# Optimization experiments

Hardware: AMD Instinct MI355X
Metric: run time of the kernel (lower is better)

Reference implementation:

```python
import jax, jax.numpy as jnp
import numpy as np

N_NODES = 32768
N_EDGES = 131072
BATCH = 512
SEQ_LEN = 1000
VOCAB = 26  # vocab_size=25 + 1 padding row
EMB = 128


def _bn(x, g, b):
    # BatchNorm1d forward with batch statistics (training-mode math), eps=1e-5
    m = x.mean(0)
    v = x.var(0)
    return g * (x - m) * jax.lax.rsqrt(v + 1e-5) + b


def _gcn(x, src, dst, W, b, n):
    deg = 1.0 + jax.ops.segment_sum(jnp.ones(src.shape[0], x.dtype), dst, num_segments=n)
    dis = jax.lax.rsqrt(deg)
    xw = x @ W
    msg = xw[src] * (dis[src] * dis[dst])[:, None]
    agg = jax.ops.segment_sum(msg, dst, num_segments=n) + xw * (dis * dis)[:, None]
    return agg + b


def _conv1d(x, k, b, pad):
    # x: [B, C_in, L], k: [C_out, C_in, K]
    y = jax.lax.conv_general_dilated(x, k, (1,), [(pad, pad)],
                                     dimension_numbers=('NCH', 'OIH', 'NCH'))
    return y + b[None, :, None]


def setup_inputs() -> dict:
    key = jax.random.key(0)
    ks = jax.random.split(key, 32)
    f = lambda i, shape, s=0.1: (jax.random.normal(ks[i], shape, dtype=jnp.float32) * s)
    inp = {
        'x': jax.random.normal(ks[0], (N_NODES, 5), dtype=jnp.float32),
        'edge_index': jax.random.randint(ks[1], (2, N_EDGES), 0, N_NODES, dtype=jnp.int32),
        'batch': jnp.sort(jax.random.randint(ks[2], (N_NODES,), 0, BATCH, dtype=jnp.int32)),
        'protein_seq': jax.random.randint(ks[3], (BATCH, SEQ_LEN), 0, VOCAB, dtype=jnp.int32),
        # GCN weights
        'W1': f(4, (5, 64)), 'b1': f(5, (64,)),
        'g1': jnp.ones((64,)), 'bt1': jnp.zeros((64,)),
        'W2': f(6, (64, 128)), 'b2': f(7, (128,)),
        'g2': jnp.ones((128,)), 'bt2': jnp.zeros((128,)),
        'W3': f(8, (128, 128)), 'b3': f(9, (128,)),
        'g3': jnp.ones((128,)), 'bt3': jnp.zeros((128,)),
        # protein embedding (row 0 = padding_idx, zeroed)
        'emb': f(10, (VOCAB, EMB)).at[0].set(0.0),
        # protein convs
        'ck1': f(11, (32, 128, 4)), 'cb1': f(12, (32,)),
        'ck2': f(13, (64, 32, 6)), 'cb2': f(14, (64,)),
        'ck3': f(15, (96, 64, 8)), 'cb3': f(16, (96,)),
        'fw1': f(17, (224, 512)), 'fb1': f(18, (512,)),
        'fw2': f(19, (512, 256)), 'fb2': f(20, (256,)),
        'fw3': f(21, (256, 1)), 'fb3': f(22, (1,)),
    }
    return inp


def reference(x, edge_index, batch, protein_seq,
              W1, b1, g1, bt1, W2, b2, g2, bt2, W3, b3, g3, bt3,
              emb, ck1, cb1, ck2, cb2, ck3, cb3,
              fw1, fb1, fw2, fb2, fw3, fb3):
    src, dst = edge_index[0], edge_index[1]
    relu = jax.nn.relu
    # Drug GNN encoder
    h = relu(_bn(_gcn(x, src, dst, W1, b1, N_NODES), g1, bt1))
    h = relu(_bn(_gcn(h, src, dst, W2, b2, N_NODES), g2, bt2))
    h = relu(_bn(_gcn(h, src, dst, W3, b3, N_NODES), g3, bt3))
    cnt = jax.ops.segment_sum(jnp.ones(N_NODES, h.dtype), batch, num_segments=BATCH)
    drug_emb = jax.ops.segment_sum(h, batch, num_segments=BATCH) / jnp.maximum(cnt, 1.0)[:, None]
    # Protein CNN encoder
    e = emb[protein_seq]                    # [B, L, 128]
    p = jnp.transpose(e, (0, 2, 1))         # [B, 128, L]
    p = relu(_conv1d(p, ck1, cb1, 1))       # [B, 32, 999]
    p = relu(_conv1d(p, ck2, cb2, 2))       # [B, 64, 998]
    p = relu(_conv1d(p, ck3, cb3, 3))       # [B, 96, 997]
    prot_emb = p.max(axis=2)                # [B, 96]
    c = jnp.concatenate([drug_emb, prot_emb], axis=1)  # [B, 224]
    c = relu(c @ fw1 + fb1)
    c = relu(c @ fw2 + fb2)
    out = (c @ fw3 + fb3)[:, 0]             # [B]
    return out
```

## Files before the change

### kernel.cpp

```cpp
#include <hip/hip_runtime.h>

#define NN 32768
#define NE 131072
#define NB 512
#define SL 1000

using bf16x8 = __attribute__((ext_vector_type(8))) short;
using f32x4  = __attribute__((ext_vector_type(4))) float;

static __device__ __forceinline__ unsigned short f2b(float f) {
  union { float f; unsigned u; } x; x.f = f;
  unsigned r = x.u + 0x7fffu + ((x.u >> 16) & 1u);
  return (unsigned short)(r >> 16);
}

static __device__ __forceinline__ void bn_from_raw(float sum, float ssq, float g, float b,
                                                   float& sc, float& sh) {
  float m = sum / 32768.f;
  float v = ssq / 32768.f - m * m;
  sc = g * rsqrtf(v + 1e-5f);
  sh = b - m * sc;
}

__global__ void k_degprep(const int* __restrict__ dst, int* __restrict__ degi,
                          const float* __restrict__ emb, const float* __restrict__ ck1,
                          const float* __restrict__ ck2, const float* __restrict__ ck3,
                          unsigned short* __restrict__ emb_bf, unsigned short* __restrict__ wt1,
                          unsigned short* __restrict__ wt2, unsigned short* __restrict__ wt3) {
  int gid = blockIdx.x * 256 + threadIdx.x;
  atomicAdd(&degi[dst[gid]], 1);
  int idx = gid;
  if (idx < 3328) {
    emb_bf[idx] = f2b(emb[idx]);
  } else if (idx < 3328 + 16384) {
    int i = idx - 3328;
    int kt = i >> 12, co = (i >> 7) & 31, ci = i & 127;
    wt1[i] = f2b(ck1[co * 512 + ci * 4 + kt]);
  } else if (idx < 3328 + 16384 + 12288) {
    int i = idx - 3328 - 16384;
    int kt = i >> 11, co = (i >> 5) & 63, ci = i & 31;
    wt2[i] = f2b(ck2[co * 192 + ci * 6 + kt]);
  } else if (idx < 3328 + 16384 + 12288 + 49152) {
    int i = idx - 3328 - 16384 - 12288;
    int kt = i / 6144, co = (i >> 6) % 96, ci = i & 63;
    wt3[i] = f2b(ck3[co * 512 + ci * 8 + kt]);
  }
}

__global__ void k_scan(const int* __restrict__ degi, int* __restrict__ base,
                       int* __restrict__ cursor, float* __restrict__ dis) {
  __shared__ int part[1024];
  int tid = threadIdx.x;
  int v[32];
  int s = 0;
  int lo = tid * 32;
#pragma unroll
  for (int i = 0; i < 32; ++i) { v[i] = degi[lo + i]; s += v[i]; }
  part[tid] = s;
  __syncthreads();
  for (int off = 1; off < 1024; off <<= 1) {
    int val = (tid >= off) ? part[tid - off] : 0;
    __syncthreads();
    part[tid] += val;
    __syncthreads();
  }
  int run = (tid > 0) ? part[tid - 1] : 0;
#pragma unroll
  for (int i = 0; i < 32; ++i) {
    base[lo + i] = run;
    cursor[lo + i] = run;
    dis[lo + i] = rsqrtf(1.0f + (float)v[i]);
    run += v[i];
  }
  if (tid == 1023) base[NN] = run;
}

__global__ void k_fill(const int* __restrict__ src, const int* __restrict__ dst,
                       int* __restrict__ cursor, unsigned short* __restrict__ csr_src, int E) {
  int e = blockIdx.x * 256 + threadIdx.x;
  if (e < E) {
    int d = dst[e];
    int pos = atomicAdd(&cursor[d], 1);
    csr_src[pos] = (unsigned short)src[e];
  }
}

__launch_bounds__(256)
__global__ void k_gfc1s(const float* __restrict__ x, const float* __restrict__ dis,
                        const int* __restrict__ base, const unsigned short* __restrict__ csr_src,
                        const float* __restrict__ W1, float* __restrict__ out,
                        float* __restrict__ st) {
  __shared__ float sW[5][64];
  __shared__ float a5[256][6];
  __shared__ float red[16][64];
  int tid = threadIdx.x;
  for (int i = tid; i < 320; i += 256) sW[i >> 6][i & 63] = W1[i];
  int n = blockIdx.x * 256 + tid;
  float dn = dis[n];
  float s2 = dn * dn;
  const float* xn = x + (long)n * 5;
  float a0 = xn[0] * s2, a1 = xn[1] * s2, a2 = xn[2] * s2, a3 = xn[3] * s2, a4 = xn[4] * s2;
  int b0 = base[n], b1 = base[n + 1];
  int sNext = (b0 < b1) ? csr_src[b0] : 0;
  for (int j = b0; j < b1; ++j) {
    int s = sNext;
    if (j + 1 < b1) sNext = csr_src[j + 1];
    float coef = dis[s] * dn;
    const float* xs = x + (long)s * 5;
    a0 += xs[0] * coef; a1 += xs[1] * coef; a2 += xs[2] * coef;
    a3 += xs[3] * coef; a4 += xs[4] * coef;
  }
  a5[tid][0] = a0; a5[tid][1] = a1; a5[tid][2] = a2; a5[tid][3] = a3; a5[tid][4] = a4;
  __syncthreads();
  int co = (tid & 15) * 4, strip = tid >> 4;
  float4 s4 = {0.f, 0.f, 0.f, 0.f}, ss4 = {0.f, 0.f, 0.f, 0.f};
  for (int i = 0; i < 16; ++i) {
    int nl = strip * 16 + i;
    long nn = (long)blockIdx.x * 256 + nl;
    float4 acc = {0.f, 0.f, 0.f, 0.f};
#pragma unroll
    for (int ci = 0; ci < 5; ++ci) {
      float av = a5[nl][ci];
      acc.x += av * sW[ci][co];     acc.y += av * sW[ci][co + 1];
      acc.z += av * sW[ci][co + 2]; acc.w += av * sW[ci][co + 3];
    }
    *(float4*)&out[nn * 64 + co] = acc;
    s4.x += acc.x; s4.y += acc.y; s4.z += acc.z; s4.w += acc.w;
    ss4.x += acc.x * acc.x; ss4.y += acc.y * acc.y;
    ss4.z += acc.z * acc.z; ss4.w += acc.w * acc.w;
  }
  *(float4*)&red[strip][co] = s4;
  __syncthreads();
  if (tid < 64) {
    float t = 0.f;
#pragma unroll
    for (int s = 0; s < 16; ++s) t += red[s][tid];
    atomicAdd(&st[tid], t);
  }
  __syncthreads();
  *(float4*)&red[strip][co] = ss4;
  __syncthreads();
  if (tid < 64) {
    float t = 0.f;
#pragma unroll
    for (int s = 0; s < 16; ++s) t += red[s][tid];
    atomicAdd(&st[64 + tid], t);
  }
}

template<int C>
__launch_bounds__(256)
__global__ void k_gbngather(const float* __restrict__ in, const float* __restrict__ dis,
                            const int* __restrict__ base, const unsigned short* __restrict__ csr_src,
                            const float* __restrict__ st, const float* __restrict__ g,
                            const float* __restrict__ bt, float* __restrict__ out) {
  constexpr int TPN = C / 4;
  int t = blockIdx.x * 256 + threadIdx.x;
  int n = t / TPN;
  int c = (t % TPN) * 4;
  float4 sum4 = *(const float4*)&st[c];
  float4 ssq4 = *(const float4*)&st[C + c];
  float4 gg = *(const float4*)&g[c];
  float4 bb = *(const float4*)&bt[c];
  float4 sc4, sh4;
  bn_from_raw(sum4.x, ssq4.x, gg.x, bb.x, sc4.x, sh4.x);
  bn_from_raw(sum4.y, ssq4.y, gg.y, bb.y, sc4.y, sh4.y);
  bn_from_raw(sum4.z, ssq4.z, gg.z, bb.z, sc4.z, sh4.z);
  bn_from_raw(sum4.w, ssq4.w, gg.w, bb.w, sc4.w, sh4.w);
  float dn = dis[n];
  float s2 = dn * dn;
  float4 a = *(const float4*)&in[(long)n * C + c];
  float4 acc;
  acc.x = fmaxf(a.x * sc4.x + sh4.x, 0.f) * s2;
  acc.y = fmaxf(a.y * sc4.y + sh4.y, 0.f) * s2;
  acc.z = fmaxf(a.z * sc4.z + sh4.z, 0.f) * s2;
  acc.w = fmaxf(a.w * sc4.w + sh4.w, 0.f) * s2;
  int b0 = base[n], b1 = base[n + 1];
  int sNext = (b0 < b1) ? csr_src[b0] : 0;
  for (int j = b0; j < b1; ++j) {
    int s = sNext;
    if (j + 1 < b1) sNext = csr_src[j + 1];
    float coef = dis[s] * dn;
    float4 vv = *(const float4*)&in[(long)s * C + c];
    acc.x += fmaxf(vv.x * sc4.x + sh4.x, 0.f) * coef;
    acc.y += fmaxf(vv.y * sc4.y + sh4.y, 0.f) * coef;
    acc.z += fmaxf(vv.z * sc4.z + sh4.z, 0.f) * coef;
    acc.w += fmaxf(vv.w * sc4.w + sh4.w, 0.f) * coef;
  }
  *(float4*)&out[(long)n * C + c] = acc;
}

template<int C_OUT, int K, int TN, bool RELU, bool BIAS, bool STATS>
__launch_bounds__(256)
__global__ void k_fc4(const float* __restrict__ in, const float* __restrict__ W,
                      const float* __restrict__ bias, float* __restrict__ out,
                      float* __restrict__ st, int N) {
  constexpr int CO4 = C_OUT / 4;
  constexpr int GPB = 256 / CO4;
  int g = blockIdx.x * GPB + threadIdx.x / CO4;
  long n0 = (long)g * TN;
  if (!STATS && n0 >= N) return;
  int co = (threadIdx.x % CO4) * 4;
  float4 acc[TN];
  float4 b4 = {0.f, 0.f, 0.f, 0.f};
  if (BIAS) b4 = *(const float4*)&bias[co];
#pragma unroll
  for (int t = 0; t < TN; ++t) acc[t] = b4;
  for (int ci = 0; ci < K; ci += 4) {
    float4 w0 = *(const float4*)&W[(long)(ci + 0) * C_OUT + co];
    float4 w1 = *(const float4*)&W[(long)(ci + 1) * C_OUT + co];
    float4 w2 = *(const float4*)&W[(long)(ci + 2) * C_OUT + co];
    float4 w3 = *(const float4*)&W[(long)(ci + 3) * C_OUT + co];
#pragma unroll
    for (int t = 0; t < TN; ++t) {
      float4 a = *(const float4*)&in[(n0 + t) * K + ci];
      acc[t].x += a.x * w0.x; acc[t].y += a.x * w0.y; acc[t].z += a.x * w0.z; acc[t].w += a.x * w0.w;
      acc[t].x += a.y * w1.x; acc[t].y += a.y * w1.y; acc[t].z += a.y * w1.z; acc[t].w += a.y * w1.w;
      acc[t].x += a.z * w2.x; acc[t].y += a.z * w2.y; acc[t].z += a.z * w2.z; acc[t].w += a.z * w2.w;
      acc[t].x += a.w * w3.x; acc[t].y += a.w * w3.y; acc[t].z += a.w * w3.z; acc[t].w += a.w * w3.w;
    }
  }
  float4 s4 = {0.f, 0.f, 0.f, 0.f}, ss4 = {0.f, 0.f, 0.f, 0.f};
#pragma unroll
  for (int t = 0; t < TN; ++t) {
    float4 o = acc[t];
    if (RELU) {
      o.x = fmaxf(o.x, 0.f); o.y = fmaxf(o.y, 0.f);
      o.z = fmaxf(o.z, 0.f); o.w = fmaxf(o.w, 0.f);
    }
    *(float4*)&out[(n0 + t) * C_OUT + co] = o;
    if (STATS) {
      s4.x += o.x; s4.y += o.y; s4.z += o.z; s4.w += o.w;
      ss4.x += o.x * o.x; ss4.y += o.y * o.y;
      ss4.z += o.z * o.z; ss4.w += o.w * o.w;
    }
  }
  if (STATS) {
    __shared__ float red2[GPB][C_OUT];
    int grp = threadIdx.x / CO4;
    *(float4*)&red2[grp][co] = s4;
    __syncthreads();
    if (threadIdx.x < C_OUT) {
      float t = 0.f;
#pragma unroll
      for (int s = 0; s < GPB; ++s) t += red2[s][threadIdx.x];
      atomicAdd(&st[threadIdx.x], t);
    }
    __syncthreads();
    *(float4*)&red2[grp][co] = ss4;
    __syncthreads();
    if (threadIdx.x < C_OUT) {
      float t = 0.f;
#pragma unroll
      for (int s = 0; s < GPB; ++s) t += red2[s][threadIdx.x];
      atomicAdd(&st[C_OUT + threadIdx.x], t);
    }
  }
}

__launch_bounds__(256)
__global__ void k_reg(const float* __restrict__ cbuf,
                      const float* __restrict__ fw1, const float* __restrict__ fb1,
                      const float* __restrict__ fw2, const float* __restrict__ fb2,
                      const float* __restrict__ fw3, const float* __restrict__ fb3,
                      float* __restrict__ out) {
  __shared__ float cin[224];
  __shared__ float h1[512];
  __shared__ float h2[256];
  __shared__ float red[4];
  int b = blockIdx.x, t = threadIdx.x;
  if (t < 224) cin[t] = cbuf[b * 224 + t];
  __syncthreads();
  {
    float a0 = fb1[t], a1 = fb1[t + 256];
    for (int ci = 0; ci < 224; ++ci) {
      float av = cin[ci];
      a0 += av * fw1[ci * 512 + t];
      a1 += av * fw1[ci * 512 + t + 256];
    }
    h1[t] = fmaxf(a0, 0.f);
    h1[t + 256] = fmaxf(a1, 0.f);
  }
  __syncthreads();
  {
    float a = fb2[t];
    for (int ci = 0; ci < 512; ++ci) a += h1[ci] * fw2[ci * 256 + t];
    h2[t] = fmaxf(a, 0.f);
  }
  __syncthreads();
  {
    float p = h2[t] * fw3[t];
#pragma unroll
    for (int off = 32; off > 0; off >>= 1) p += __shfl_down(p, off, 64);
    if ((t & 63) == 0) red[t >> 6] = p;
    __syncthreads();
    if (t == 0) out[b] = red[0] + red[1] + red[2] + red[3] + fb3[0];
  }
}

__launch_bounds__(256)
__global__ void conv_mfma(const int* __restrict__ seq, const unsigned short* __restrict__ emb_bf,
                          const unsigned short* __restrict__ wt1g, const float* __restrict__ cb1,
                          const unsigned short* __restrict__ wt2g, const float* __restrict__ cb2,
                          const unsigned short* __restrict__ wt3g, const float* __restrict__ cb3,
                          const float* __restrict__ agg, const float* __restrict__ st3,
                          const float* __restrict__ g3, const float* __restrict__ bt3,
                          const int* __restrict__ batch, float* __restrict__ outmax) {
  __shared__ __align__(16) unsigned short s_w[17408];
  __shared__ __align__(16) unsigned short s_c1[152][40];
  __shared__ __align__(16) unsigned short s_c2[144][72];
  __shared__ int s_tok[152];
  __shared__ int s_max[96];

  int tid = threadIdx.x;
  int b = blockIdx.y;

  if (blockIdx.x == 8) {
    __shared__ int s_lo, s_hi;
    if (tid == 0) {
      int lo = 0, hi = NN;
      while (lo < hi) { int m = (lo + hi) >> 1; if (batch[m] < b) lo = m + 1; else hi = m; }
      s_lo = lo;
      hi = NN;
      while (lo < hi) { int m = (lo + hi) >> 1; if (batch[m] <= b) lo = m + 1; else hi = m; }
      s_hi = lo;
    }
    __syncthreads();
    if (tid < 128) {
      int lo = s_lo, hi = s_hi, c = tid;
      float sc, sh;
      bn_from_raw(st3[c], st3[128 + c], g3[c], bt3[c], sc, sh);
      float s = 0.f;
      for (int n = lo; n < hi; ++n) s += fmaxf(agg[(long)n * 128 + c] * sc + sh, 0.f);
      outmax[b * 224 + c] = s / fmaxf((float)(hi - lo), 1.0f);
    }
    return;
  }

  int t0 = blockIdx.x * 128;

  if (tid < 96) s_max[tid] = 0;
  if (tid < 152) {
    int p = t0 - 6 + tid;
    s_tok[tid] = (p >= 0 && p < SL) ? seq[b * SL + p] : 0;
  }
  if (tid < 160) ((int*)&s_c1[144][0])[tid] = 0;

  for (int c = 0; c < 8; ++c) {
    int ch = c * 256 + tid;
    int row = ch >> 4, col = (ch & 15) * 8;
    *(bf16x8*)&s_w[row * 136 + col] = *(const bf16x8*)(wt1g + ch * 8);
  }
  __syncthreads();

  int lane = tid & 63, wave = tid >> 6;
  int l15 = lane & 15, quad = lane >> 4;

  {
    int mt0 = wave, mt1 = wave + 4;
    f32x4 acc[2][2];
#pragma unroll
    for (int nt = 0; nt < 2; ++nt) {
      float bv = cb1[nt * 16 + l15];
      acc[0][nt] = (f32x4){bv, bv, bv, bv};
      acc[1][nt] = (f32x4){bv, bv, bv, bv};
    }
    for (int kt = 0; kt < 4; ++kt) {
      const unsigned short* e0 = emb_bf + s_tok[mt0 * 16 + l15 + kt] * 128 + quad * 8;
      const unsigned short* e1 = emb_bf + s_tok[mt1 * 16 + l15 + kt] * 128 + quad * 8;
#pragma unroll
      for (int cb = 0; cb < 4; ++cb) {
        bf16x8 a0 = *(const bf16x8*)(e0 + cb * 32);
        bf16x8 a1 = *(const bf16x8*)(e1 + cb * 32);
#pragma unroll
        for (int nt = 0; nt < 2; ++nt) {
          bf16x8 bf = *(const bf16x8*)&s_w[(kt * 32 + nt * 16 + l15) * 136 + cb * 32 + quad * 8];
          acc[0][nt] = __builtin_amdgcn_mfma_f32_16x16x32_bf16(a0, bf, acc[0][nt], 0, 0, 0);
          acc[1][nt] = __builtin_amdgcn_mfma_f32_16x16x32_bf16(a1, bf, acc[1][nt], 0, 0, 0);
        }
      }
    }
#pragma unroll
    for (int mb = 0; mb < 2; ++mb) {
      int mt = mb ? mt1 : mt0;
#pragma unroll
      for (int nt = 0; nt < 2; ++nt) {
        int co = nt * 16 + l15;
#pragma unroll
        for (int r = 0; r < 4; ++r) {
          int m = mt * 16 + quad * 4 + r;
          int l1 = t0 - 5 + m;
          unsigned short hv = f2b(fmaxf(acc[mb][nt][r], 0.f));
          s_c1[m][co] = (l1 >= 0 && l1 < 999) ? hv : (unsigned short)0;
        }
      }
    }
    if (wave == 0) {
      f32x4 acc8[2];
#pragma unroll
      for (int nt = 0; nt < 2; ++nt) {
        float bv = cb1[nt * 16 + l15];
        acc8[nt] = (f32x4){bv, bv, bv, bv};
      }
      for (int kt = 0; kt < 4; ++kt) {
        const unsigned short* e0 = emb_bf + s_tok[128 + l15 + kt] * 128 + quad * 8;
#pragma unroll
        for (int cb = 0; cb < 4; ++cb) {
          bf16x8 a0 = *(const bf16x8*)(e0 + cb * 32);
#pragma unroll
          for (int nt = 0; nt < 2; ++nt) {
            bf16x8 bf = *(const bf16x8*)&s_w[(kt * 32 + nt * 16 + l15) * 136 + cb * 32 + quad * 8];
            acc8[nt] = __builtin_amdgcn_mfma_f32_16x16x32_bf16(a0, bf, acc8[nt], 0, 0, 0);
          }
        }
      }
#pragma unroll
      for (int nt = 0; nt < 2; ++nt) {
        int co = nt * 16 + l15;
#pragma unroll
        for (int r = 0; r < 4; ++r) {
          int m = 128 + quad * 4 + r;
          int l1 = t0 - 5 + m;
          unsigned short hv = f2b(fmaxf(acc8[nt][r], 0.f));
          s_c1[m][co] = (l1 >= 0 && l1 < 999) ? hv : (unsigned short)0;
        }
      }
    }
  }

  {
    bf16x8 w2t[6];
#pragma unroll
    for (int c = 0; c < 6; ++c) w2t[c] = *(const bf16x8*)(wt2g + (c * 256 + tid) * 8);
    __syncthreads();
#pragma unroll
    for (int c = 0; c < 6; ++c) {
      int ch = c * 256 + tid;
      int row = ch >> 2, col = (ch & 3) * 8;
      *(bf16x8*)&s_w[row * 40 + col] = w2t[c];
    }
    __syncthreads();
  }

  {
    int mt0 = wave, mt1 = wave + 4;
    f32x4 acc[2][4];
#pragma unroll
    for (int nt = 0; nt < 4; ++nt) {
      float bv = cb2[nt * 16 + l15];
      acc[0][nt] = (f32x4){bv, bv, bv, bv};
      acc[1][nt] = (f32x4){bv, bv, bv, bv};
    }
    for (int kt = 0; kt < 6; ++kt) {
      bf16x8 a0 = *(const bf16x8*)&s_c1[mt0 * 16 + l15 + kt][quad * 8];
      bf16x8 a1 = *(const bf16x8*)&s_c1[mt1 * 16 + l15 + kt][quad * 8];
#pragma unroll
      for (int nt = 0; nt < 4; ++nt) {
        bf16x8 bf = *(const bf16x8*)&s_w[(kt * 64 + nt * 16 + l15) * 40 + quad * 8];
        acc[0][nt] = __builtin_amdgcn_mfma_f32_16x16x32_bf16(a0, bf, acc[0][nt], 0, 0, 0);
        acc[1][nt] = __builtin_amdgcn_mfma_f32_16x16x32_bf16(a1, bf, acc[1][nt], 0, 0, 0);
      }
    }
#pragma unroll
    for (int mb = 0; mb < 2; ++mb) {
      int mt = mb ? mt1 : mt0;
#pragma unroll
      for (int nt = 0; nt < 4; ++nt) {
        int co = nt * 16 + l15;
#pragma unroll
        for (int r = 0; r < 4; ++r) {
          int m = mt * 16 + quad * 4 + r;
          int l2 = t0 - 3 + m;
          unsigned short hv = f2b(fmaxf(acc[mb][nt][r], 0.f));
          s_c2[m][co] = (l2 >= 0 && l2 < 998) ? hv : (unsigned short)0;
        }
      }
    }
    if (wave == 0) {
      f32x4 acc8[4];
#pragma unroll
      for (int nt = 0; nt < 4; ++nt) {
        float bv = cb2[nt * 16 + l15];
        acc8[nt] = (f32x4){bv, bv, bv, bv};
      }
      for (int kt = 0; kt < 6; ++kt) {
        bf16x8 a0 = *(const bf16x8*)&s_c1[128 + l15 + kt][quad * 8];
#pragma unroll
        for (int nt = 0; nt < 4; ++nt) {
          bf16x8 bf = *(const bf16x8*)&s_w[(kt * 64 + nt * 16 + l15) * 40 + quad * 8];
          acc8[nt] = __builtin_amdgcn_mfma_f32_16x16x32_bf16(a0, bf, acc8[nt], 0, 0, 0);
        }
      }
#pragma unroll
      for (int nt = 0; nt < 4; ++nt) {
        int co = nt * 16 + l15;
#pragma unroll
        for (int r = 0; r < 4; ++r) {
          int m = 128 + quad * 4 + r;
          int l2 = t0 - 3 + m;
          unsigned short hv = f2b(fmaxf(acc8[nt][r], 0.f));
          s_c2[m][co] = (l2 >= 0 && l2 < 998) ? hv : (unsigned short)0;
        }
      }
    }
  }

  {
    bf16x8 w3t[3];
#pragma unroll
    for (int c = 0; c < 3; ++c) w3t[c] = *(const bf16x8*)(wt3g + (c * 256 + tid) * 8);
    __syncthreads();
#pragma unroll
    for (int c = 0; c < 3; ++c) {
      int ch = c * 256 + tid;
      int row = ch >> 3, col = (ch & 7) * 8;
      *(bf16x8*)&s_w[row * 72 + col] = w3t[c];
    }
    __syncthreads();
  }

  {
    int mt0 = wave, mt1 = wave + 4;
    f32x4 acc[2][6];
#pragma unroll
    for (int nt = 0; nt < 6; ++nt) {
      float bv = cb3[nt * 16 + l15];
      acc[0][nt] = (f32x4){bv, bv, bv, bv};
      acc[1][nt] = (f32x4){bv, bv, bv, bv};
    }
    for (int kt = 0; kt < 8; ++kt) {
      bf16x8 w3t[3];
      if (kt < 7) {
#pragma unroll
        for (int c = 0; c < 3; ++c)
          w3t[c] = *(const bf16x8*)(wt3g + ((kt + 1) * 768 + c * 256 + tid) * 8);
      }
      int bo = (kt & 1) * 6912;
#pragma unroll
      for (int cb = 0; cb < 2; ++cb) {
        bf16x8 a0 = *(const bf16x8*)&s_c2[mt0 * 16 + l15 + kt][cb * 32 + quad * 8];
        bf16x8 a1 = *(const bf16x8*)&s_c2[mt1 * 16 + l15 + kt][cb * 32 + quad * 8];
#pragma unroll
        for (int nt = 0; nt < 6; ++nt) {
          bf16x8 bf = *(const bf16x8*)&s_w[bo + (nt * 16 + l15) * 72 + cb * 32 + quad * 8];
          acc[0][nt] = __builtin_amdgcn_mfma_f32_16x16x32_bf16(a0, bf, acc[0][nt], 0, 0, 0);
          acc[1][nt] = __builtin_amdgcn_mfma_f32_16x16x32_bf16(a1, bf, acc[1][nt], 0, 0, 0);
        }
      }
      if (kt < 7) {
        int bo2 = ((kt + 1) & 1) * 6912;
#pragma unroll
        for (int c = 0; c < 3; ++c) {
          int ch = c * 256 + tid;
          int row = ch >> 3, col = (ch & 7) * 8;
          *(bf16x8*)&s_w[bo2 + row * 72 + col] = w3t[c];
        }
      }
      __syncthreads();
    }
#pragma unroll
    for (int nt = 0; nt < 6; ++nt) {
      int co = nt * 16 + l15;
      float mx = 0.f;
#pragma unroll
      for (int mb = 0; mb < 2; ++mb) {
        int mt = mb ? mt1 : mt0;
#pragma unroll
        for (int r = 0; r < 4; ++r) {
          int l3 = t0 + mt * 16 + quad * 4 + r;
          if (l3 < 997) mx = fmaxf(mx, acc[mb][nt][r]);
        }
      }
      atomicMax(&s_max[co], __float_as_int(mx));
    }
  }
  __syncthreads();
  if (tid < 96) atomicMax((int*)&outmax[b * 224 + 128 + tid], s_max[tid]);
}

extern "C" void kernel_launch(void* const* d_in, const int* in_sizes, int n_in,
                              void* d_out, int out_size, void* d_ws, size_t ws_size,
                              hipStream_t stream) {
  (void)in_sizes; (void)n_in; (void)out_size; (void)ws_size;
  const float* x = (const float*)d_in[0];
  const int* ei = (const int*)d_in[1];
  const int* batch = (const int*)d_in[2];
  const int* seq = (const int*)d_in[3];
  const float* W1 = (const float*)d_in[4];
  const float* g1 = (const float*)d_in[6];
  const float* bt1 = (const float*)d_in[7];
  const float* W2 = (const float*)d_in[8];
  const float* g2 = (const float*)d_in[10];
  const float* bt2 = (const float*)d_in[11];
  const float* W3 = (const float*)d_in[12];
  const float* g3 = (const float*)d_in[14];
  const float* bt3 = (const float*)d_in[15];
  const float* emb = (const float*)d_in[16];
  const float* ck1 = (const float*)d_in[17];
  const float* cb1 = (const float*)d_in[18];
  const float* ck2 = (const float*)d_in[19];
  const float* cb2 = (const float*)d_in[20];
  const float* ck3 = (const float*)d_in[21];
  const float* cb3 = (const float*)d_in[22];
  const float* fw1 = (const float*)d_in[23];
  const float* fb1 = (const float*)d_in[24];
  const float* fw2 = (const float*)d_in[25];
  const float* fb2 = (const float*)d_in[26];
  const float* fw3 = (const float*)d_in[27];
  const float* fb3 = (const float*)d_in[28];
  const int* src = ei;
  const int* dst = ei + NE;

  float* ws = (float*)d_ws;
  float* bufA = ws;
  float* bufB = ws + 4194304;
  float* dis = ws + 8388608;
  float* stats = ws + 8421376;
  float* cbuf = ws + 8422032;
  int* degi = (int*)(ws + 8536720);
  int* base = degi + NN;
  int* cursor = base + NN + 1;
  unsigned short* csr_src = (unsigned short*)(cursor + NN);
  unsigned short* emb_bf = (unsigned short*)(ws + 8700564);
  unsigned short* wt1 = emb_bf + 3328;
  unsigned short* wt2 = wt1 + 16384;
  unsigned short* wt3 = wt2 + 12288;
  float* out = (float*)d_out;

  hipMemsetAsync(stats, 0, (656 + 114688 + 32768) * sizeof(float), stream);

  k_degprep<<<NE / 256, 256, 0, stream>>>(dst, degi, emb, ck1, ck2, ck3, emb_bf, wt1, wt2, wt3);
  k_scan<<<1, 1024, 0, stream>>>(degi, base, cursor, dis);
  k_fill<<<NE / 256, 256, 0, stream>>>(src, dst, cursor, csr_src, NE);

  k_gfc1s<<<NN / 256, 256, 0, stream>>>(x, dis, base, csr_src, W1, bufA, stats);
  k_gbngather<64><<<NN * 16 / 256, 256, 0, stream>>>(bufA, dis, base, csr_src, stats, g1, bt1, bufB);
  k_fc4<128, 64, 4, false, false, true><<<1024, 256, 0, stream>>>(bufB, W2, nullptr, bufA, stats + 128, NN);
  k_gbngather<128><<<NN * 32 / 256, 256, 0, stream>>>(bufA, dis, base, csr_src, stats + 128, g2, bt2, bufB);
  k_fc4<128, 128, 4, false, false, true><<<1024, 256, 0, stream>>>(bufB, W3, nullptr, bufA, stats + 384, NN);

  conv_mfma<<<dim3(9, NB), 256, 0, stream>>>(seq, emb_bf, wt1, cb1, wt2, cb2, wt3, cb3,
                                             bufA, stats + 384, g3, bt3, batch, cbuf);

  k_reg<<<NB, 256, 0, stream>>>(cbuf, fw1, fb1, fw2, fb2, fw3, fb3, out);
}
```

Measured before the change: 464.4 us.

## Shrink conv LDS with XOR swizzles and double-buffered conv1 weights for occupancy

Replaces padded shared-memory arrays with XOR-swizzled unpadded layouts for weights and intermediate activations, and streams conv1 weights per tap through a double buffer instead of loading all at once. The smaller LDS footprint plus a launch bound of 3 blocks per CU aims to raise occupancy while keeping LDS reads conflict-free. It also merges the tail-tile conv1 work into the main tap loop. The added per-tap barriers and register caps may cost some latency or cause spills.

```diff
diff --git a/kernel.cpp b/kernel.cpp
--- a/kernel.cpp
+++ b/kernel.cpp
@@ -298,7 +298,7 @@
   }
 }
 
-__launch_bounds__(256)
+__launch_bounds__(256, 3)
 __global__ void conv_mfma(const int* __restrict__ seq, const unsigned short* __restrict__ emb_bf,
                           const unsigned short* __restrict__ wt1g, const float* __restrict__ cb1,
                           const unsigned short* __restrict__ wt2g, const float* __restrict__ cb2,
@@ -306,9 +306,9 @@
                           const float* __restrict__ agg, const float* __restrict__ st3,
                           const float* __restrict__ g3, const float* __restrict__ bt3,
                           const int* __restrict__ batch, float* __restrict__ outmax) {
-  __shared__ __align__(16) unsigned short s_w[17408];
-  __shared__ __align__(16) unsigned short s_c1[152][40];
-  __shared__ __align__(16) unsigned short s_c2[144][72];
+  __shared__ __align__(16) unsigned short s_w[12288];
+  __shared__ __align__(16) unsigned short s_c1[4864];
+  __shared__ __align__(16) unsigned short s_c2[9216];
   __shared__ int s_tok[152];
   __shared__ int s_max[96];
 
@@ -344,12 +344,12 @@
     int p = t0 - 6 + tid;
     s_tok[tid] = (p >= 0 && p < SL) ? seq[b * SL + p] : 0;
   }
-  if (tid < 160) ((int*)&s_c1[144][0])[tid] = 0;
-
-  for (int c = 0; c < 8; ++c) {
-    int ch = c * 256 + tid;
-    int row = ch >> 4, col = (ch & 15) * 8;
-    *(bf16x8*)&s_w[row * 136 + col] = *(const bf16x8*)(wt1g + ch * 8);
+  if (tid < 128) ((int*)(s_c1 + 144 * 32))[tid] = 0;
+
+  {
+    int v0 = tid, v1 = tid + 256;
+    *(bf16x8*)&s_w[(v0 >> 4) * 128 + ((((v0 >> 4) ^ v0) & 15) << 3)] = *(const bf16x8*)(wt1g + v0 * 8);
+    *(bf16x8*)&s_w[(v1 >> 4) * 128 + ((((v1 >> 4) ^ v1) & 15) << 3)] = *(const bf16x8*)(wt1g + v1 * 8);
   }
   __syncthreads();
 
@@ -358,14 +358,23 @@
 
   {
     int mt0 = wave, mt1 = wave + 4;
-    f32x4 acc[2][2];
+    f32x4 acc0[2], acc1[2], acc2[2];
 #pragma unroll
     for (int nt = 0; nt < 2; ++nt) {
       float bv = cb1[nt * 16 + l15];
-      acc[0][nt] = (f32x4){bv, bv, bv, bv};
-      acc[1][nt] = (f32x4){bv, bv, bv, bv};
+      acc0[nt] = (f32x4){bv, bv, bv, bv};
+      acc1[nt] = (f32x4){bv, bv, bv, bv};
+      acc2[nt] = (f32x4){bv, bv, bv, bv};
     }
     for (int kt = 0; kt < 4; ++kt) {
+      int bo = (kt & 1) * 4096;
+      if (kt < 3) {
+        int bo2 = 4096 - bo;
+        const unsigned short* wsrc = wt1g + (kt + 1) * 4096;
+        int v0 = tid, v1 = tid + 256;
+        *(bf16x8*)&s_w[bo2 + (v0 >> 4) * 128 + ((((v0 >> 4) ^ v0) & 15) << 3)] = *(const bf16x8*)(wsrc + v0 * 8);
+        *(bf16x8*)&s_w[bo2 + (v1 >> 4) * 128 + ((((v1 >> 4) ^ v1) & 15) << 3)] = *(const bf16x8*)(wsrc + v1 * 8);
+      }
       const unsigned short* e0 = emb_bf + s_tok[mt0 * 16 + l15 + kt] * 128 + quad * 8;
       const unsigned short* e1 = emb_bf + s_tok[mt1 * 16 + l15 + kt] * 128 + quad * 8;
 #pragma unroll
@@ -374,46 +383,45 @@
         bf16x8 a1 = *(const bf16x8*)(e1 + cb * 32);
 #pragma unroll
         for (int nt = 0; nt < 2; ++nt) {
-          bf16x8 bf = *(const bf16x8*)&s_w[(kt * 32 + nt * 16 + l15) * 136 + cb * 32 + quad * 8];
-          acc[0][nt] = __builtin_amdgcn_mfma_f32_16x16x32_bf16(a0, bf, acc[0][nt], 0, 0, 0);
-          acc[1][nt] = __builtin_amdgcn_mfma_f32_16x16x32_bf16(a1, bf, acc[1][nt], 0, 0, 0);
-        }
-      }
-    }
-#pragma unroll
-    for (int mb = 0; mb < 2; ++mb) {
-      int mt = mb ? mt1 : mt0;
-#pragma unroll
-      for (int nt = 0; nt < 2; ++nt) {
-        int co = nt * 16 + l15;
-#pragma unroll
-        for (int r = 0; r < 4; ++r) {
-          int m = mt * 16 + quad * 4 + r;
+          bf16x8 bf = *(const bf16x8*)&s_w[bo + (nt * 16 + l15) * 128 + (((cb * 4 + quad) ^ l15) << 3)];
+          acc0[nt] = __builtin_amdgcn_mfma_f32_16x16x32_bf16(a0, bf, acc0[nt], 0, 0, 0);
+          acc1[nt] = __builtin_amdgcn_mfma_f32_16x16x32_bf16(a1, bf, acc1[nt], 0, 0, 0);
+        }
+      }
+      if (wave == 0) {
+        const unsigned short* e2 = emb_bf + s_tok[128 + l15 + kt] * 128 + quad * 8;
+#pragma unroll
+        for (int cb = 0; cb < 4; ++cb) {
+          bf16x8 a2 = *(const bf16x8*)(e2 + cb * 32);
+#pragma unroll
+          for (int nt = 0; nt < 2; ++nt) {
+            bf16x8 bf = *(const bf16x8*)&s_w[bo + (nt * 16 + l15) * 128 + (((cb * 4 + quad) ^ l15) << 3)];
+            acc2[nt] = __builtin_amdgcn_mfma_f32_16x16x32_bf16(a2, bf, acc2[nt], 0, 0, 0);
+          }
+        }
+      }
+      __syncthreads();
+    }
+#pragma unroll
+    for (int nt = 0; nt < 2; ++nt) {
+      int co = nt * 16 + l15;
+#pragma unroll
+      for (int r = 0; r < 4; ++r) {
+        {
+          int m = mt0 * 16 + quad * 4 + r;
           int l1 = t0 - 5 + m;
-          unsigned short hv = f2b(fmaxf(acc[mb][nt][r], 0.f));
-          s_c1[m][co] = (l1 >= 0 && l1 < 999) ? hv : (unsigned short)0;
+          unsigned short hv = f2b(fmaxf(acc0[nt][r], 0.f));
+          s_c1[m * 32 + ((((co >> 3) ^ m) & 3) << 3) + (co & 7)] = (l1 >= 0 && l1 < 999) ? hv : (unsigned short)0;
+        }
+        {
+          int m = mt1 * 16 + quad * 4 + r;
+          int l1 = t0 - 5 + m;
+          unsigned short hv = f2b(fmaxf(acc1[nt][r], 0.f));
+          s_c1[m * 32 + ((((co >> 3) ^ m) & 3) << 3) + (co & 7)] = (l1 >= 0 && l1 < 999) ? hv : (unsigned short)0;
         }
       }
     }
     if (wave == 0) {
-      f32x4 acc8[2];
-#pragma unroll
-      for (int nt = 0; nt < 2; ++nt) {
-        float bv = cb1[nt * 16 + l15];
-        acc8[nt] = (f32x4){bv, bv, bv, bv};
-      }
-      for (int kt = 0; kt < 4; ++kt) {
-        const unsigned short* e0 = emb_bf + s_tok[128 + l15 + kt] * 128 + quad * 8;
-#pragma unroll
-        for (int cb = 0; cb < 4; ++cb) {
-          bf16x8 a0 = *(const bf16x8*)(e0 + cb * 32);
-#pragma unroll
-          for (int nt = 0; nt < 2; ++nt) {
-            bf16x8 bf = *(const bf16x8*)&s_w[(kt * 32 + nt * 16 + l15) * 136 + cb * 32 + quad * 8];
-            acc8[nt] = __builtin_amdgcn_mfma_f32_16x16x32_bf16(a0, bf, acc8[nt], 0, 0, 0);
-          }
-        }
-      }
 #pragma unroll
       for (int nt = 0; nt < 2; ++nt) {
         int co = nt * 16 + l15;
@@ -421,8 +429,8 @@
         for (int r = 0; r < 4; ++r) {
           int m = 128 + quad * 4 + r;
           int l1 = t0 - 5 + m;
-          unsigned short hv = f2b(fmaxf(acc8[nt][r], 0.f));
-          s_c1[m][co] = (l1 >= 0 && l1 < 999) ? hv : (unsigned short)0;
+          unsigned short hv = f2b(fmaxf(acc2[nt][r], 0.f));
+          s_c1[m * 32 + ((((co >> 3) ^ m) & 3) << 3) + (co & 7)] = (l1 >= 0 && l1 < 999) ? hv : (unsigned short)0;
         }
       }
     }
@@ -432,12 +440,11 @@
     bf16x8 w2t[6];
 #pragma unroll
     for (int c = 0; c < 6; ++c) w2t[c] = *(const bf16x8*)(wt2g + (c * 256 + tid) * 8);
-    __syncthreads();
 #pragma unroll
     for (int c = 0; c < 6; ++c) {
       int ch = c * 256 + tid;
-      int row = ch >> 2, col = (ch & 3) * 8;
-      *(bf16x8*)&s_w[row * 40 + col] = w2t[c];
+      int row = ch >> 2;
+      *(bf16x8*)&s_w[row * 32 + (((row ^ ch) & 3) << 3)] = w2t[c];
     }
     __syncthreads();
   }
@@ -452,11 +459,13 @@
       acc[1][nt] = (f32x4){bv, bv, bv, bv};
     }
     for (int kt = 0; kt < 6; ++kt) {
-      bf16x8 a0 = *(const bf16x8*)&s_c1[mt0 * 16 + l15 + kt][quad * 8];
-      bf16x8 a1 = *(const bf16x8*)&s_c1[mt1 * 16 + l15 + kt][quad * 8];
+      int r0 = mt0 * 16 + l15 + kt, r1 = mt1 * 16 + l15 + kt;
+      bf16x8 a0 = *(const bf16x8*)&s_c1[r0 * 32 + (((quad ^ r0) & 3) << 3)];
+      bf16x8 a1 = *(const bf16x8*)&s_c1[r1 * 32 + (((quad ^ r1) & 3) << 3)];
 #pragma unroll
       for (int nt = 0; nt < 4; ++nt) {
-        bf16x8 bf = *(const bf16x8*)&s_w[(kt * 64 + nt * 16 + l15) * 40 + quad * 8];
+        int wr = kt * 64 + nt * 16 + l15;
+        bf16x8 bf = *(const bf16x8*)&s_w[wr * 32 + (((quad ^ wr) & 3) << 3)];
         acc[0][nt] = __builtin_amdgcn_mfma_f32_16x16x32_bf16(a0, bf, acc[0][nt], 0, 0, 0);
         acc[1][nt] = __builtin_amdgcn_mfma_f32_16x16x32_bf16(a1, bf, acc[1][nt], 0, 0, 0);
       }
@@ -472,7 +481,7 @@
           int m = mt * 16 + quad * 4 + r;
           int l2 = t0 - 3 + m;
           unsigned short hv = f2b(fmaxf(acc[mb][nt][r], 0.f));
-          s_c2[m][co] = (l2 >= 0 && l2 < 998) ? hv : (unsigned short)0;
+          s_c2[m * 64 + ((((co >> 3) ^ m) & 7) << 3) + (co & 7)] = (l2 >= 0 && l2 < 998) ? hv : (unsigned short)0;
         }
       }
     }
@@ -484,10 +493,12 @@
         acc8[nt] = (f32x4){bv, bv, bv, bv};
       }
       for (int kt = 0; kt < 6; ++kt) {
-        bf16x8 a0 = *(const bf16x8*)&s_c1[128 + l15 + kt][quad * 8];
+        int r0 = 128 + l15 + kt;
+        bf16x8 a0 = *(const bf16x8*)&s_c1[r0 * 32 + (((quad ^ r0) & 3) << 3)];
 #pragma unroll
         for (int nt = 0; nt < 4; ++nt) {
-          bf16x8 bf = *(const bf16x8*)&s_w[(kt * 64 + nt * 16 + l15) * 40 + quad * 8];
+          int wr = kt * 64 + nt * 16 + l15;
+          bf16x8 bf = *(const bf16x8*)&s_w[wr * 32 + (((quad ^ wr) & 3) << 3)];
           acc8[nt] = __builtin_amdgcn_mfma_f32_16x16x32_bf16(a0, bf, acc8[nt], 0, 0, 0);
         }
       }
@@ -499,7 +510,7 @@
           int m = 128 + quad * 4 + r;
           int l2 = t0 - 3 + m;
           unsigned short hv = f2b(fmaxf(acc8[nt][r], 0.f));
-          s_c2[m][co] = (l2 >= 0 && l2 < 998) ? hv : (unsigned short)0;
+          s_c2[m * 64 + ((((co >> 3) ^ m) & 7) << 3) + (co & 7)] = (l2 >= 0 && l2 < 998) ? hv : (unsigned short)0;
         }
       }
     }
@@ -513,8 +524,8 @@
 #pragma unroll
     for (int c = 0; c < 3; ++c) {
       int ch = c * 256 + tid;
-      int row = ch >> 3, col = (ch & 7) * 8;
-      *(bf16x8*)&s_w[row * 72 + col] = w3t[c];
+      int row = ch >> 3;
+      *(bf16x8*)&s_w[row * 64 + (((row ^ ch) & 7) << 3)] = w3t[c];
     }
     __syncthreads();
   }
@@ -535,25 +546,27 @@
         for (int c = 0; c < 3; ++c)
           w3t[c] = *(const bf16x8*)(wt3g + ((kt + 1) * 768 + c * 256 + tid) * 8);
       }
-      int bo = (kt & 1) * 6912;
+      int bo = (kt & 1) * 6144;
+      int ra0 = mt0 * 16 + l15 + kt, ra1 = mt1 * 16 + l15 + kt;
 #pragma unroll
       for (int cb = 0; cb < 2; ++cb) {
-        bf16x8 a0 = *(const bf16x8*)&s_c2[mt0 * 16 + l15 + kt][cb * 32 + quad * 8];
-        bf16x8 a1 = *(const bf16x8*)&s_c2[mt1 * 16 + l15 + kt][cb * 32 + quad * 8];
+        bf16x8 a0 = *(const bf16x8*)&s_c2[ra0 * 64 + ((((cb * 4 + quad) ^ ra0) & 7) << 3)];
+        bf16x8 a1 = *(const bf16x8*)&s_c2[ra1 * 64 + ((((cb * 4 + quad) ^ ra1) & 7) << 3)];
 #pragma unroll
         for (int nt = 0; nt < 6; ++nt) {
-          bf16x8 bf = *(const bf16x8*)&s_w[bo + (nt * 16 + l15) * 72 + cb * 32 + quad * 8];
+          int wr = nt * 16 + l15;
+          bf16x8 bf = *(const bf16x8*)&s_w[bo + wr * 64 + ((((cb * 4 + quad) ^ wr) & 7) << 3)];
           acc[0][nt] = __builtin_amdgcn_mfma_f32_16x16x32_bf16(a0, bf, acc[0][nt], 0, 0, 0);
           acc[1][nt] = __builtin_amdgcn_mfma_f32_16x16x32_bf16(a1, bf, acc[1][nt], 0, 0, 0);
         }
       }
       if (kt < 7) {
-        int bo2 = ((kt + 1) & 1) * 6912;
+        int bo2 = 6144 - bo;
 #pragma unroll
         for (int c = 0; c < 3; ++c) {
           int ch = c * 256 + tid;
-          int row = ch >> 3, col = (ch & 7) * 8;
-          *(bf16x8*)&s_w[bo2 + row * 72 + col] = w3t[c];
+          int row = ch >> 3;
+          *(bf16x8*)&s_w[bo2 + row * 64 + (((row ^ ch) & 7) << 3)] = w3t[c];
         }
       }
       __syncthreads();
```

Result: faster. 431.2 us (-7.2%).
